# Optimization experiments

Hardware: AMD Instinct MI355X
Metric: run time of the kernel (lower is better)

The kernel has to match this reference:

```python
import jax, jax.numpy as jnp
import numpy as np

Y_DIM = 2
Z_DIM = 128
EPS = 1e-08


def setup_inputs() -> dict:
    key = jax.random.key(0)
    k1, k2, k3, k4 = jax.random.split(key, 4)
    b, n, m, x_dim = 8, 1024, 2048, 1
    c = Y_DIM + 1
    x = jax.random.normal(k1, (b, n, x_dim), dtype=jnp.float32)
    y = jax.random.normal(k2, (b, n, Y_DIM), dtype=jnp.float32)
    t = jax.random.normal(k3, (b, m, x_dim), dtype=jnp.float32)
    # learned params
    sigma = jnp.zeros((c,), dtype=jnp.float32)  # log(length_scale=1) = 0
    W = jax.random.normal(k4, (Z_DIM, c), dtype=jnp.float32) * 0.05
    b_fc = jnp.zeros((Z_DIM,), dtype=jnp.float32)
    return {"x": x, "y": y, "t": t, "sigma": sigma, "W": W, "b_fc": b_fc}


def reference(x, y, t, sigma, W, b_fc):
    # rbf_kernel: diff summed over x_dim -> (b, n, m)
    diff = jnp.sum(t[:, None, :, :] - x[:, :, None, :], axis=-1)  # (b,n,m)
    scale = jnp.exp(sigma)  # (c,)
    # kernel: (b,n,m,c)
    kernel = jnp.exp(-0.5 * (diff[..., None] / scale) ** 2)
    # z = [density=1, y] broadcast-multiplied by kernel, summed over n
    b_, n_, _ = y.shape
    feats = jnp.concatenate([jnp.ones((b_, n_, 1), dtype=y.dtype), y], axis=-1)  # (b,n,c)
    z = jnp.einsum("bnc,bnmc->bmc", feats, kernel)  # (b,m,c)
    density = z[..., :1]
    normalized = z[..., 1:] / (density + EPS)
    z = jnp.concatenate([density, normalized], axis=-1)  # (b,m,c)
    return z @ W.T + b_fc  # (b,m,z_dim)
```

## Files before the change

kernel.cpp:

```cpp
#include <hip/hip_runtime.h>
#include <hip/hip_bf16.h>

constexpr int B  = 8;
constexpr int N  = 1024;
constexpr int M  = 2048;
constexpr int ZD = 128;
constexpr int JPW = 2;
constexpr int JPB = 4 * JPW;
constexpr float EPS = 1e-8f;
constexpr float LOG2E = 1.4426950408889634f;

__global__ __launch_bounds__(256, 8) void encoder_fused(
    const float* __restrict__ x,
    const float* __restrict__ y,
    const float* __restrict__ t,
    const float* __restrict__ sigma,
    const float* __restrict__ W,
    const float* __restrict__ bfc,
    float* __restrict__ out)
{
    __shared__ float sx[N];
    __shared__ float sy1[N];
    __shared__ float sy2[N];

    const int blk  = blockIdx.x;
    const int b    = blk / (M / JPB);
    const int jt   = blk % (M / JPB);
    const int tid  = threadIdx.x;
    const int wave = tid >> 6;
    const int lane = tid & 63;

    for (int i = tid; i < N; i += 256) {
        sx[i] = x[b * N + i];
        float2 yv = reinterpret_cast<const float2*>(y)[b * N + i];
        sy1[i] = yv.x;
        sy2[i] = yv.y;
    }
    __syncthreads();

    const float s0 = sigma[0], s1 = sigma[1], s2 = sigma[2];
    const float q0 = -0.5f * LOG2E * __builtin_amdgcn_exp2f(-2.0f * s0 * LOG2E);
    const float q1 = -0.5f * LOG2E * __builtin_amdgcn_exp2f(-2.0f * s1 * LOG2E);
    const float q2 = -0.5f * LOG2E * __builtin_amdgcn_exp2f(-2.0f * s2 * LOG2E);

    const int j0 = jt * JPB + wave * JPW;
    const float ta = t[b * M + j0];
    const float tb = t[b * M + j0 + 1];

    float z0a = 0.f, z1a = 0.f, z2a = 0.f;
    float z0b = 0.f, z1b = 0.f, z2b = 0.f;

    if (s0 == s1 && s1 == s2) {
#pragma unroll
        for (int k = 0; k < N / 64; ++k) {
            const int i = k * 64 + lane;
            const float xi = sx[i], y1 = sy1[i], y2 = sy2[i];
            const float da = ta - xi, db = tb - xi;
            const float ea = __builtin_amdgcn_exp2f(da * da * q0);
            const float eb = __builtin_amdgcn_exp2f(db * db * q0);
            z0a += ea;  z1a = fmaf(y1, ea, z1a);  z2a = fmaf(y2, ea, z2a);
            z0b += eb;  z1b = fmaf(y1, eb, z1b);  z2b = fmaf(y2, eb, z2b);
        }
    } else {
#pragma unroll
        for (int k = 0; k < N / 64; ++k) {
            const int i = k * 64 + lane;
            const float xi = sx[i], y1 = sy1[i], y2 = sy2[i];
            const float da = ta - xi, db = tb - xi;
            const float da2 = da * da, db2 = db * db;
            z0a += __builtin_amdgcn_exp2f(da2 * q0);
            z1a = fmaf(y1, __builtin_amdgcn_exp2f(da2 * q1), z1a);
            z2a = fmaf(y2, __builtin_amdgcn_exp2f(da2 * q2), z2a);
            z0b += __builtin_amdgcn_exp2f(db2 * q0);
            z1b = fmaf(y1, __builtin_amdgcn_exp2f(db2 * q1), z1b);
            z2b = fmaf(y2, __builtin_amdgcn_exp2f(db2 * q2), z2b);
        }
    }

#pragma unroll
    for (int off = 32; off; off >>= 1) {
        z0a += __shfl_xor(z0a, off);
        z1a += __shfl_xor(z1a, off);
        z2a += __shfl_xor(z2a, off);
        z0b += __shfl_xor(z0b, off);
        z1b += __shfl_xor(z1b, off);
        z2b += __shfl_xor(z2b, off);
    }

    const float inva = 1.0f / (z0a + EPS);
    const float a1 = z1a * inva, a2 = z2a * inva;
    const float invb = 1.0f / (z0b + EPS);
    const float b1 = z1b * invb, b2 = z2b * invb;

    const int k0 = lane * 2;
    const float w00 = W[k0 * 3 + 0], w01 = W[k0 * 3 + 1], w02 = W[k0 * 3 + 2];
    const float w10 = W[(k0 + 1) * 3 + 0], w11 = W[(k0 + 1) * 3 + 1], w12 = W[(k0 + 1) * 3 + 2];
    const float bf0 = bfc[k0], bf1 = bfc[k0 + 1];

    float2 oa, ob;
    oa.x = fmaf(z0a, w00, fmaf(a1, w01, fmaf(a2, w02, bf0)));
    oa.y = fmaf(z0a, w10, fmaf(a1, w11, fmaf(a2, w12, bf1)));
    ob.x = fmaf(z0b, w00, fmaf(b1, w01, fmaf(b2, w02, bf0)));
    ob.y = fmaf(z0b, w10, fmaf(b1, w11, fmaf(b2, w12, bf1)));

    reinterpret_cast<float2*>(out)[(size_t)(b * M + j0) * (ZD / 2) + lane]       = oa;
    reinterpret_cast<float2*>(out)[(size_t)(b * M + j0 + 1) * (ZD / 2) + lane]   = ob;
}

extern "C" void kernel_launch(void* const* d_in, const int* in_sizes, int n_in,
                              void* d_out, int out_size, void* d_ws, size_t ws_size,
                              hipStream_t stream) {
    const float* x     = (const float*)d_in[0];
    const float* y     = (const float*)d_in[1];
    const float* t     = (const float*)d_in[2];
    const float* sigma = (const float*)d_in[3];
    const float* W     = (const float*)d_in[4];
    const float* bfc   = (const float*)d_in[5];
    float* out = (float*)d_out;

    dim3 grid(B * (M / JPB));
    encoder_fused<<<grid, 256, 0, stream>>>(x, y, t, sigma, W, bfc, out);
}
```

Before: 72.59 us.

## Assign one output row per 32-lane group with float4 LDS reads

Each block still handles 8 output rows, but each row now goes to a 32-lane half-wave instead of each wave handling two rows. Each lane reads float4 vectors of x and y from LDS, so it needs fewer LDS instructions and has more independent exp work per load. The shuffle reduction shrinks to 5 steps over 32 lanes and the output is written as float4. Staging into shared memory uses float4 global loads plus a deinterleave of y. In exchange, each x/y load now feeds only one t value rather than two, which may raise LDS traffic per exp. The partial-wave shuffle and the float4 LDS reads may also cause bank conflicts.

```diff
diff --git a/kernel.cpp b/kernel.cpp
--- a/kernel.cpp
+++ b/kernel.cpp
@@ -1,12 +1,9 @@
 #include <hip/hip_runtime.h>
-#include <hip/hip_bf16.h>
 
 constexpr int B  = 8;
 constexpr int N  = 1024;
 constexpr int M  = 2048;
 constexpr int ZD = 128;
-constexpr int JPW = 2;
-constexpr int JPB = 4 * JPW;
 constexpr float EPS = 1e-8f;
 constexpr float LOG2E = 1.4426950408889634f;
 
@@ -19,92 +16,109 @@
     const float* __restrict__ bfc,
     float* __restrict__ out)
 {
-    __shared__ float sx[N];
-    __shared__ float sy1[N];
-    __shared__ float sy2[N];
+    __shared__ __align__(16) float sx[N];
+    __shared__ __align__(16) float sy1[N];
+    __shared__ __align__(16) float sy2[N];
 
-    const int blk  = blockIdx.x;
-    const int b    = blk / (M / JPB);
-    const int jt   = blk % (M / JPB);
-    const int tid  = threadIdx.x;
-    const int wave = tid >> 6;
-    const int lane = tid & 63;
+    const int blk = blockIdx.x;
+    const int b   = blk >> 8;
+    const int jt  = blk & 255;
+    const int tid = threadIdx.x;
+    const int l32 = tid & 31;
+    const int grp = tid >> 5;
 
-    for (int i = tid; i < N; i += 256) {
-        sx[i] = x[b * N + i];
-        float2 yv = reinterpret_cast<const float2*>(y)[b * N + i];
-        sy1[i] = yv.x;
-        sy2[i] = yv.y;
+    {
+        const float4* x4 = reinterpret_cast<const float4*>(x + b * N);
+        reinterpret_cast<float4*>(sx)[tid] = x4[tid];
+
+        const float4* y4 = reinterpret_cast<const float4*>(y + (size_t)b * N * 2);
+        const float4 v0 = y4[tid];
+        const float4 v1 = y4[tid + 256];
+        *reinterpret_cast<float2*>(&sy1[2 * tid])         = make_float2(v0.x, v0.z);
+        *reinterpret_cast<float2*>(&sy2[2 * tid])         = make_float2(v0.y, v0.w);
+        *reinterpret_cast<float2*>(&sy1[2 * (tid + 256)]) = make_float2(v1.x, v1.z);
+        *reinterpret_cast<float2*>(&sy2[2 * (tid + 256)]) = make_float2(v1.y, v1.w);
     }
-    __syncthreads();
 
     const float s0 = sigma[0], s1 = sigma[1], s2 = sigma[2];
     const float q0 = -0.5f * LOG2E * __builtin_amdgcn_exp2f(-2.0f * s0 * LOG2E);
     const float q1 = -0.5f * LOG2E * __builtin_amdgcn_exp2f(-2.0f * s1 * LOG2E);
     const float q2 = -0.5f * LOG2E * __builtin_amdgcn_exp2f(-2.0f * s2 * LOG2E);
 
-    const int j0 = jt * JPB + wave * JPW;
-    const float ta = t[b * M + j0];
-    const float tb = t[b * M + j0 + 1];
+    const int   j  = jt * 8 + grp;
+    const float tj = t[b * M + j];
 
-    float z0a = 0.f, z1a = 0.f, z2a = 0.f;
-    float z0b = 0.f, z1b = 0.f, z2b = 0.f;
+    __syncthreads();
+
+    float z0 = 0.f, z1 = 0.f, z2 = 0.f;
 
     if (s0 == s1 && s1 == s2) {
 #pragma unroll
-        for (int k = 0; k < N / 64; ++k) {
-            const int i = k * 64 + lane;
-            const float xi = sx[i], y1 = sy1[i], y2 = sy2[i];
-            const float da = ta - xi, db = tb - xi;
-            const float ea = __builtin_amdgcn_exp2f(da * da * q0);
-            const float eb = __builtin_amdgcn_exp2f(db * db * q0);
-            z0a += ea;  z1a = fmaf(y1, ea, z1a);  z2a = fmaf(y2, ea, z2a);
-            z0b += eb;  z1b = fmaf(y1, eb, z1b);  z2b = fmaf(y2, eb, z2b);
+        for (int c = 0; c < N / 128; ++c) {
+            const int i = c * 128 + l32 * 4;
+            const float4 xv  = *reinterpret_cast<const float4*>(&sx[i]);
+            const float4 y1v = *reinterpret_cast<const float4*>(&sy1[i]);
+            const float4 y2v = *reinterpret_cast<const float4*>(&sy2[i]);
+            float d, e;
+            d = tj - xv.x; e = __builtin_amdgcn_exp2f(d * d * q0);
+            z0 += e; z1 = fmaf(y1v.x, e, z1); z2 = fmaf(y2v.x, e, z2);
+            d = tj - xv.y; e = __builtin_amdgcn_exp2f(d * d * q0);
+            z0 += e; z1 = fmaf(y1v.y, e, z1); z2 = fmaf(y2v.y, e, z2);
+            d = tj - xv.z; e = __builtin_amdgcn_exp2f(d * d * q0);
+            z0 += e; z1 = fmaf(y1v.z, e, z1); z2 = fmaf(y2v.z, e, z2);
+            d = tj - xv.w; e = __builtin_amdgcn_exp2f(d * d * q0);
+            z0 += e; z1 = fmaf(y1v.w, e, z1); z2 = fmaf(y2v.w, e, z2);
         }
     } else {
 #pragma unroll
-        for (int k = 0; k < N / 64; ++k) {
-            const int i = k * 64 + lane;
-            const float xi = sx[i], y1 = sy1[i], y2 = sy2[i];
-            const float da = ta - xi, db = tb - xi;
-            const float da2 = da * da, db2 = db * db;
-            z0a += __builtin_amdgcn_exp2f(da2 * q0);
-            z1a = fmaf(y1, __builtin_amdgcn_exp2f(da2 * q1), z1a);
-            z2a = fmaf(y2, __builtin_amdgcn_exp2f(da2 * q2), z2a);
-            z0b += __builtin_amdgcn_exp2f(db2 * q0);
-            z1b = fmaf(y1, __builtin_amdgcn_exp2f(db2 * q1), z1b);
-            z2b = fmaf(y2, __builtin_amdgcn_exp2f(db2 * q2), z2b);
+        for (int c = 0; c < N / 128; ++c) {
+            const int i = c * 128 + l32 * 4;
+            const float4 xv  = *reinterpret_cast<const float4*>(&sx[i]);
+            const float4 y1v = *reinterpret_cast<const float4*>(&sy1[i]);
+            const float4 y2v = *reinterpret_cast<const float4*>(&sy2[i]);
+            float d, d2;
+            d = tj - xv.x; d2 = d * d;
+            z0 += __builtin_amdgcn_exp2f(d2 * q0);
+            z1 = fmaf(y1v.x, __builtin_amdgcn_exp2f(d2 * q1), z1);
+            z2 = fmaf(y2v.x, __builtin_amdgcn_exp2f(d2 * q2), z2);
+            d = tj - xv.y; d2 = d * d;
+            z0 += __builtin_amdgcn_exp2f(d2 * q0);
+            z1 = fmaf(y1v.y, __builtin_amdgcn_exp2f(d2 * q1), z1);
+            z2 = fmaf(y2v.y, __builtin_amdgcn_exp2f(d2 * q2), z2);
+            d = tj - xv.z; d2 = d * d;
+            z0 += __builtin_amdgcn_exp2f(d2 * q0);
+            z1 = fmaf(y1v.z, __builtin_amdgcn_exp2f(d2 * q1), z1);
+            z2 = fmaf(y2v.z, __builtin_amdgcn_exp2f(d2 * q2), z2);
+            d = tj - xv.w; d2 = d * d;
+            z0 += __builtin_amdgcn_exp2f(d2 * q0);
+            z1 = fmaf(y1v.w, __builtin_amdgcn_exp2f(d2 * q1), z1);
+            z2 = fmaf(y2v.w, __builtin_amdgcn_exp2f(d2 * q2), z2);
         }
     }
 
 #pragma unroll
-    for (int off = 32; off; off >>= 1) {
-        z0a += __shfl_xor(z0a, off);
-        z1a += __shfl_xor(z1a, off);
-        z2a += __shfl_xor(z2a, off);
-        z0b += __shfl_xor(z0b, off);
-        z1b += __shfl_xor(z1b, off);
-        z2b += __shfl_xor(z2b, off);
+    for (int off = 16; off; off >>= 1) {
+        z0 += __shfl_xor(z0, off);
+        z1 += __shfl_xor(z1, off);
+        z2 += __shfl_xor(z2, off);
     }
 
-    const float inva = 1.0f / (z0a + EPS);
-    const float a1 = z1a * inva, a2 = z2a * inva;
-    const float invb = 1.0f / (z0b + EPS);
-    const float b1 = z1b * invb, b2 = z2b * invb;
+    const float inv = 1.0f / (z0 + EPS);
+    const float a1 = z1 * inv, a2 = z2 * inv;
 
-    const int k0 = lane * 2;
-    const float w00 = W[k0 * 3 + 0], w01 = W[k0 * 3 + 1], w02 = W[k0 * 3 + 2];
-    const float w10 = W[(k0 + 1) * 3 + 0], w11 = W[(k0 + 1) * 3 + 1], w12 = W[(k0 + 1) * 3 + 2];
-    const float bf0 = bfc[k0], bf1 = bfc[k0 + 1];
+    const float4* W4 = reinterpret_cast<const float4*>(W);
+    const float4 wa = W4[l32 * 3 + 0];
+    const float4 wb = W4[l32 * 3 + 1];
+    const float4 wc = W4[l32 * 3 + 2];
+    const float4 bf = reinterpret_cast<const float4*>(bfc)[l32];
 
-    float2 oa, ob;
-    oa.x = fmaf(z0a, w00, fmaf(a1, w01, fmaf(a2, w02, bf0)));
-    oa.y = fmaf(z0a, w10, fmaf(a1, w11, fmaf(a2, w12, bf1)));
-    ob.x = fmaf(z0b, w00, fmaf(b1, w01, fmaf(b2, w02, bf0)));
-    ob.y = fmaf(z0b, w10, fmaf(b1, w11, fmaf(b2, w12, bf1)));
+    float4 o;
+    o.x = fmaf(z0, wa.x, fmaf(a1, wa.y, fmaf(a2, wa.z, bf.x)));
+    o.y = fmaf(z0, wa.w, fmaf(a1, wb.x, fmaf(a2, wb.y, bf.y)));
+    o.z = fmaf(z0, wb.z, fmaf(a1, wb.w, fmaf(a2, wc.x, bf.z)));
+    o.w = fmaf(z0, wc.y, fmaf(a1, wc.z, fmaf(a2, wc.w, bf.w)));
 
-    reinterpret_cast<float2*>(out)[(size_t)(b * M + j0) * (ZD / 2) + lane]       = oa;
-    reinterpret_cast<float2*>(out)[(size_t)(b * M + j0 + 1) * (ZD / 2) + lane]   = ob;
+    reinterpret_cast<float4*>(out)[(size_t)(b * M + j) * (ZD / 4) + l32] = o;
 }
 
 extern "C" void kernel_launch(void* const* d_in, const int* in_sizes, int n_in,
@@ -118,6 +132,6 @@
     const float* bfc   = (const float*)d_in[5];
     float* out = (float*)d_out;
 
-    dim3 grid(B * (M / JPB));
+    dim3 grid(B * (M / 8));
     encoder_fused<<<grid, 256, 0, stream>>>(x, y, t, sigma, W, bfc, out);
 }
```

Result: faster. 70.13 us (-3.4%).
